# Optimization experiments

Measured on AMD Instinct MI355X. Metric: run time of the kernel, lower is better.

The kernel has to match this reference:

```python
import jax, jax.numpy as jnp
import numpy as np

LN_EPS = 1e-5      # torch.nn.LayerNorm default
NORM_EPS = 1e-12   # torch F.normalize default


def _layernorm(x, gamma, beta):
    mu = jnp.mean(x, axis=-1, keepdims=True)
    var = jnp.mean(jnp.square(x - mu), axis=-1, keepdims=True)
    return (x - mu) * jax.lax.rsqrt(var + LN_EPS) * gamma + beta


def _l2norm(x):
    # normalize over last (embedding) axis, matching F.normalize(dim=1) on [B,E,1,N]
    n = jnp.sqrt(jnp.sum(jnp.square(x), axis=-1, keepdims=True))
    return x / jnp.maximum(n, NORM_EPS)


def setup_inputs() -> dict:
    key = jax.random.key(0)
    ks = jax.random.split(key, 4)
    B, N, C, E = 8, 4096, 768, 768
    x = jax.random.normal(ks[0], (B, N, C), dtype=jnp.float32)
    w_qkv = jax.random.normal(ks[1], (C, 3 * E), dtype=jnp.float32) * (1.0 / np.sqrt(C))
    w_proj = jax.random.normal(ks[2], (E, C), dtype=jnp.float32) * (1.0 / np.sqrt(E))
    ln_in_g = jnp.ones((C,), jnp.float32)
    ln_in_b = jnp.zeros((C,), jnp.float32)
    ln_out_g = jnp.ones((E,), jnp.float32)
    ln_out_b = jnp.zeros((E,), jnp.float32)
    return {"x": x, "w_qkv": w_qkv, "w_proj": w_proj,
            "ln_in_g": ln_in_g, "ln_in_b": ln_in_b,
            "ln_out_g": ln_out_g, "ln_out_b": ln_out_b}


def reference(x, w_qkv, w_proj, ln_in_g, ln_in_b, ln_out_g, ln_out_b):
    # x: [B, N, C]
    h = _layernorm(x, ln_in_g, ln_in_b)
    qkv = h @ w_qkv                                  # [B, N, 3E]
    q, k, v = jnp.split(qkv, 3, axis=-1)             # each [B, N, E]
    phi_q = _l2norm(q)                               # per-token L2 over E
    phi_k = _l2norm(k)
    kv = jnp.sum(phi_k * v, axis=1)                  # [B, E] (sum over tokens N)
    attn = phi_q * kv[:, None, :]                    # [B, N, E]
    out = _layernorm(attn, ln_out_g, ln_out_b) @ w_proj  # [B, N, C]
    return out
```

## Files before the change

kernel.cpp:

```cpp
#include <hip/hip_runtime.h>
#include <hip/hip_bf16.h>
#include <cstdint>

typedef __bf16 bf16;
typedef __bf16 bf16x4 __attribute__((ext_vector_type(4)));
typedef __bf16 bf16x8 __attribute__((ext_vector_type(8)));
typedef float f32x4 __attribute__((ext_vector_type(4)));

#define GK 768
#define LN_EPS 1e-5f
#define NORM_EPS 1e-12f

__device__ __forceinline__ void gl_lds16(const void* g, void* l) {
  __builtin_amdgcn_global_load_lds(
      (__attribute__((address_space(1))) uint32_t*)(uintptr_t)g,
      (__attribute__((address_space(3))) uint32_t*)(uintptr_t)l,
      16, 0, 0);
}

__device__ __forceinline__ void blockReduce2w3(float& s, float& ss, float* sm) {
  #pragma unroll
  for (int o = 32; o > 0; o >>= 1) {
    s  += __shfl_down(s, o, 64);
    ss += __shfl_down(ss, o, 64);
  }
  int wave = threadIdx.x >> 6, lane = threadIdx.x & 63;
  if (lane == 0) { sm[wave] = s; sm[3 + wave] = ss; }
  __syncthreads();
  s  = sm[0] + sm[1] + sm[2];
  ss = sm[3] + sm[4] + sm[5];
  __syncthreads();
}

__global__ __launch_bounds__(256) void transpose_cvt(const float* __restrict__ w,
                                                     bf16* __restrict__ wt,
                                                     int R, int Ncols) {
  __shared__ float tile[32][33];
  int tx = threadIdx.x & 31, ty = threadIdx.x >> 5;
  int c0 = blockIdx.x * 32, r0 = blockIdx.y * 32;
  #pragma unroll
  for (int i = 0; i < 32; i += 8)
    tile[ty + i][tx] = w[(size_t)(r0 + ty + i) * Ncols + (c0 + tx)];
  __syncthreads();
  #pragma unroll
  for (int i = 0; i < 32; i += 8)
    wt[(size_t)(c0 + ty + i) * R + (r0 + tx)] = (bf16)tile[tx][ty + i];
}

__global__ __launch_bounds__(192) void ln_in_kernel(const float* __restrict__ x,
                                                    const float* __restrict__ g,
                                                    const float* __restrict__ b,
                                                    bf16* __restrict__ h) {
  __shared__ float sm[6];
  int row = blockIdx.x, t = threadIdx.x;
  const float* xr = x + (size_t)row * 768;
  float4 v = ((const float4*)xr)[t];
  float s  = v.x + v.y + v.z + v.w;
  float ss = v.x * v.x + v.y * v.y + v.z * v.z + v.w * v.w;
  blockReduce2w3(s, ss, sm);
  float mu  = s * (1.0f / 768.0f);
  float inv = rsqrtf(ss * (1.0f / 768.0f) - mu * mu + LN_EPS);
  float4 gg = ((const float4*)g)[t];
  float4 bb = ((const float4*)b)[t];
  bf16x4 o;
  o[0] = (bf16)((v.x - mu) * inv * gg.x + bb.x);
  o[1] = (bf16)((v.y - mu) * inv * gg.y + bb.y);
  o[2] = (bf16)((v.z - mu) * inv * gg.z + bb.z);
  o[3] = (bf16)((v.w - mu) * inv * gg.w + bb.w);
  ((bf16x4*)(h + (size_t)row * 768))[t] = o;
}


#define SWZ(x) ((x) ^ ((((x) >> 7) & 7) << 4))

#define BAR __builtin_amdgcn_s_barrier()
#define VMC(n) asm volatile("s_waitcnt vmcnt(" #n ")" ::: "memory")
#define PRIO1 __builtin_amdgcn_s_setprio(1)
#define PRIO0 __builtin_amdgcn_s_setprio(0)

#define LDA1(base, mh, i, ks) \
  af[i][ks] = *(const bf16x8*)((base) + SWZ((wm * 128 + ((mh) * 4 + (i)) * 16 + llo) * 128 + (ks) * 64 + lhi * 16))
#define RD_A(base, mh) do { \
  LDA1(base, mh, 0, 0); LDA1(base, mh, 1, 0); LDA1(base, mh, 2, 0); LDA1(base, mh, 3, 0); \
  LDA1(base, mh, 0, 1); LDA1(base, mh, 1, 1); LDA1(base, mh, 2, 1); LDA1(base, mh, 3, 1); } while (0)

#define LDB1(base, n, ks) \
  bf[n][ks] = *(const bf16x8*)((base) + SWZ(((((n) >> 1) * 128 + wn * 32 + ((n) & 1) * 16 + llo) * 128 + (ks) * 64 + lhi * 16)))
#define RD_B01(base) do { LDB1(base, 0, 0); LDB1(base, 1, 0); LDB1(base, 0, 1); LDB1(base, 1, 1); } while (0)
#define RD_B23(base) do { LDB1(base, 2, 0); LDB1(base, 3, 0); LDB1(base, 2, 1); LDB1(base, 3, 1); } while (0)

#define MF1(mh, nh, i, jn, ks) \
  acc[(mh) * 4 + (i)][(nh) * 2 + (jn)] = __builtin_amdgcn_mfma_f32_16x16x32_bf16( \
      af[i][ks], bf[(nh) * 2 + (jn)][ks], acc[(mh) * 4 + (i)][(nh) * 2 + (jn)], 0, 0, 0)
#define MF8(mh, nh, ks) do { \
  MF1(mh, nh, 0, 0, ks); MF1(mh, nh, 0, 1, ks); MF1(mh, nh, 1, 0, ks); MF1(mh, nh, 1, 1, ks); \
  MF1(mh, nh, 2, 0, ks); MF1(mh, nh, 2, 1, ks); MF1(mh, nh, 3, 0, ks); MF1(mh, nh, 3, 1, ks); } while (0)
#define MFQ(mh, nh) do { PRIO1; MF8(mh, nh, 0); MF8(mh, nh, 1); PRIO0; } while (0)

#define STA(b, q, kt) gl_lds16(A + srcA[q] + (kt) * 64, &As_[b][(q) * 4096 + wave * 512])
#define STB(b, q, kt) gl_lds16(Bt + srcB[q] + (kt) * 64, &Bs_[b][(q) * 4096 + wave * 512])

template <bool OUT_BF16>
__global__ __launch_bounds__(512, 2) void gemm8p(const bf16* __restrict__ A,
                                                 const bf16* __restrict__ Bt,
                                                 void* __restrict__ Cv,
                                                 int Nn, int NBN) {
  __shared__ __align__(16) bf16 As_[2][16384];
  __shared__ __align__(16) bf16 Bs_[2][16384];
  const int tid = threadIdx.x;
  const int wave = tid >> 6, lane = tid & 63;
  const int llo = lane & 15, lhi = lane >> 4;
  const int wm = wave >> 2, wn = wave & 3;

  const int nwg = gridDim.x, bid = blockIdx.x;
  const int wg = (bid & 7) * (nwg >> 3) + (bid >> 3);
  const int rb = wg / NBN, cb = wg - rb * NBN;
  const int brow = rb * 256, bcol = cb * 256;

  uint32_t srcA[4], srcB[4];
  #pragma unroll
  for (int q = 0; q < 4; ++q) {
    int d = q * 8192 + tid * 16;
    int a = SWZ(d);
    int r = a >> 7, c = (a & 127) >> 1;
    srcA[q] = (uint32_t)(brow + r) * GK + c;
    int nh = r >> 7, wnn = (r >> 5) & 3, r32 = r & 31;
    srcB[q] = (uint32_t)(bcol + wnn * 64 + nh * 32 + r32) * GK + c;
  }

  f32x4 acc[8][4];
  #pragma unroll
  for (int m = 0; m < 8; ++m)
    #pragma unroll
    for (int n = 0; n < 4; ++n) acc[m][n] = (f32x4){0.f, 0.f, 0.f, 0.f};

  bf16x8 af[4][2], bf[4][2];
  const char* As0 = (const char*)&As_[0][0];
  const char* As1 = (const char*)&As_[1][0];
  const char* Bs0 = (const char*)&Bs_[0][0];
  const char* Bs1 = (const char*)&Bs_[1][0];

  STA(0, 0, 0); STA(0, 1, 0); STA(0, 2, 0); STA(0, 3, 0);
  STB(0, 0, 0); STB(0, 1, 0); STB(0, 2, 0); STB(0, 3, 0);
  STA(1, 0, 1); STA(1, 2, 1); STB(1, 0, 1); STB(1, 1, 1);
  VMC(4);
  BAR;

  for (int j = 0; j < 6; ++j) {
    const int t1 = 2 * j + 1, t2 = 2 * j + 2, t3 = 2 * j + 3;
    RD_A(As0, 0); RD_B01(Bs0); RD_B23(Bs0);
    STA(1, 1, t1); STA(1, 3, t1);
    BAR;
    MFQ(0, 0);
    BAR;
    STB(1, 2, t1); STB(1, 3, t1);
    BAR;
    MFQ(0, 1);
    BAR;
    RD_A(As0, 1);
    STA(0, 0, t2); STA(0, 2, t2);
    BAR;
    MFQ(1, 0);
    BAR;
    STB(0, 0, t2); STB(0, 1, t2);
    BAR;
    MFQ(1, 1);
    VMC(4);
    BAR;
    RD_A(As1, 0); RD_B01(Bs1); RD_B23(Bs1);
    STA(0, 1, t2); STA(0, 3, t2);
    BAR;
    MFQ(0, 0);
    BAR;
    STB(0, 2, t2); STB(0, 3, t2);
    BAR;
    MFQ(0, 1);
    BAR;
    RD_A(As1, 1);
    STA(1, 0, t3); STA(1, 2, t3);
    BAR;
    MFQ(1, 0);
    BAR;
    STB(1, 0, t3); STB(1, 1, t3);
    BAR;
    MFQ(1, 1);
    VMC(4);
    BAR;
  }

  #pragma unroll
  for (int m = 0; m < 8; ++m) {
    #pragma unroll
    for (int n = 0; n < 4; ++n) {
      int row = brow + wm * 128 + m * 16 + lhi * 4;
      int col = bcol + wn * 64 + n * 16 + llo;
      #pragma unroll
      for (int r2 = 0; r2 < 4; ++r2) {
        if (OUT_BF16)
          ((bf16*)Cv)[(size_t)(row + r2) * Nn + col] = (bf16)acc[m][n][r2];
        else
          ((float*)Cv)[(size_t)(row + r2) * Nn + col] = acc[m][n][r2];
      }
    }
  }
}

__global__ __launch_bounds__(256) void kv_partial(const bf16* __restrict__ qkv,
                                                  float* __restrict__ kvp) {
  __shared__ float sm[4][768];
  int b = blockIdx.x >> 5, chunk = blockIdx.x & 31;
  int wave = threadIdx.x >> 6, lane = threadIdx.x & 63;
  const bf16* base = qkv + ((size_t)(b * 4096 + chunk * 128 + wave * 32)) * 2304;
  float acc[3][4] = {};
  for (int i = 0; i < 32; ++i) {
    const bf16* kr = base + (size_t)i * 2304 + 768;
    const bf16* vr = kr + 768;
    bf16x4 k4[3], v4[3];
    #pragma unroll
    for (int c = 0; c < 3; ++c) {
      k4[c] = *(const bf16x4*)(kr + c * 256 + lane * 4);
      v4[c] = *(const bf16x4*)(vr + c * 256 + lane * 4);
    }
    float ssk = 0.f;
    #pragma unroll
    for (int c = 0; c < 3; ++c)
      #pragma unroll
      for (int j = 0; j < 4; ++j) { float kf = (float)k4[c][j]; ssk += kf * kf; }
    #pragma unroll
    for (int off = 32; off > 0; off >>= 1) ssk += __shfl_xor(ssk, off, 64);
    float wi = 1.0f / fmaxf(sqrtf(ssk), NORM_EPS);
    #pragma unroll
    for (int c = 0; c < 3; ++c)
      #pragma unroll
      for (int j = 0; j < 4; ++j)
        acc[c][j] += (float)k4[c][j] * (float)v4[c][j] * wi;
  }
  #pragma unroll
  for (int c = 0; c < 3; ++c)
    #pragma unroll
    for (int j = 0; j < 4; ++j)
      sm[wave][c * 256 + lane * 4 + j] = acc[c][j];
  __syncthreads();
  int t = threadIdx.x;
  #pragma unroll
  for (int c = 0; c < 3; ++c) {
    int e = c * 256 + t;
    kvp[(size_t)blockIdx.x * 768 + e] = sm[0][e] + sm[1][e] + sm[2][e] + sm[3][e];
  }
}

__global__ __launch_bounds__(256) void kv_reduce(const float* __restrict__ kvp,
                                                 float* __restrict__ kv) {
  int i = blockIdx.x * 256 + threadIdx.x;
  int b = i / 768, e = i - b * 768;
  float s = 0.f;
  #pragma unroll
  for (int c = 0; c < 32; ++c) s += kvp[(size_t)(b * 32 + c) * 768 + e];
  kv[i] = s;
}

__global__ __launch_bounds__(192) void attn_ln_kernel(const bf16* __restrict__ qkv,
                                                      const float* __restrict__ kv,
                                                      const float* __restrict__ g,
                                                      const float* __restrict__ b,
                                                      bf16* __restrict__ a) {
  __shared__ float sm[6];
  int row = blockIdx.x, t = threadIdx.x;
  int bt = row >> 12;
  const bf16* qr = qkv + (size_t)row * 2304;
  bf16x4 q4 = ((const bf16x4*)qr)[t];
  float q0 = (float)q4[0], q1 = (float)q4[1], q2 = (float)q4[2], q3 = (float)q4[3];
  float sq = q0 * q0 + q1 * q1 + q2 * q2 + q3 * q3, dummy = 0.f;
  blockReduce2w3(sq, dummy, sm);
  float iq = 1.0f / fmaxf(sqrtf(sq), NORM_EPS);
  float4 kv4 = ((const float4*)(kv + bt * 768))[t];
  float4 av;
  av.x = q0 * iq * kv4.x;
  av.y = q1 * iq * kv4.y;
  av.z = q2 * iq * kv4.z;
  av.w = q3 * iq * kv4.w;
  float s  = av.x + av.y + av.z + av.w;
  float ss = av.x * av.x + av.y * av.y + av.z * av.z + av.w * av.w;
  blockReduce2w3(s, ss, sm);
  float mu  = s * (1.0f / 768.0f);
  float inv = rsqrtf(ss * (1.0f / 768.0f) - mu * mu + LN_EPS);
  float4 gg = ((const float4*)g)[t];
  float4 bb = ((const float4*)b)[t];
  bf16x4 o;
  o[0] = (bf16)((av.x - mu) * inv * gg.x + bb.x);
  o[1] = (bf16)((av.y - mu) * inv * gg.y + bb.y);
  o[2] = (bf16)((av.z - mu) * inv * gg.z + bb.z);
  o[3] = (bf16)((av.w - mu) * inv * gg.w + bb.w);
  ((bf16x4*)(a + (size_t)row * 768))[t] = o;
}

extern "C" void kernel_launch(void* const* d_in, const int* in_sizes, int n_in,
                              void* d_out, int out_size, void* d_ws, size_t ws_size,
                              hipStream_t stream) {
  const float* x      = (const float*)d_in[0];
  const float* w_qkv  = (const float*)d_in[1];
  const float* w_proj = (const float*)d_in[2];
  const float* g_in   = (const float*)d_in[3];
  const float* b_in   = (const float*)d_in[4];
  const float* g_out  = (const float*)d_in[5];
  const float* b_out  = (const float*)d_in[6];

  char* ws = (char*)d_ws;
  bf16*  wqkvt  = (bf16*)(ws);
  bf16*  wprojt = (bf16*)(ws + 3538944);
  bf16*  h      = (bf16*)(ws + 4718592);
  bf16*  qkv    = (bf16*)(ws + 55050240);
  float* kvp    = (float*)(ws + 206045184);
  float* kv     = (float*)(ws + 206831616);

  transpose_cvt<<<dim3(2304 / 32, 768 / 32), 256, 0, stream>>>(w_qkv, wqkvt, 768, 2304);
  transpose_cvt<<<dim3(768 / 32, 768 / 32), 256, 0, stream>>>(w_proj, wprojt, 768, 768);
  ln_in_kernel<<<32768, 192, 0, stream>>>(x, g_in, b_in, h);
  gemm8p<true><<<128 * 9, 512, 0, stream>>>(h, wqkvt, (void*)qkv, 2304, 9);
  kv_partial<<<256, 256, 0, stream>>>(qkv, kvp);
  kv_reduce<<<24, 256, 0, stream>>>(kvp, kv);
  attn_ln_kernel<<<32768, 192, 0, stream>>>(qkv, kv, g_out, b_out, h);
  gemm8p<false><<<128 * 3, 512, 0, stream>>>(h, wprojt, d_out, 768, 3);
}
```

Baseline: 292.3 us.

## Replace 256x256 GEMM tile with simpler 128x128 tile and double-buffered pipeline

Swaps the 512-thread 256x256-tile GEMM, with its finely interleaved quarter-step load/compute schedule, for a 256-thread 128x128-tile kernel. Each K-step reads all fragments, runs all 32 MFMAs, then stages the next full tile into the freed buffer. This gives a simpler schedule with fewer barriers and more workgroups for better CU fill. In exchange each tile gets less data reuse, so global and LDS traffic per FLOP rises, and load latency is less finely overlapped.

Result: faster. 268.9 us (-8.0%).

```diff
diff --git a/kernel.cpp b/kernel.cpp
--- a/kernel.cpp
+++ b/kernel.cpp
@@ -78,59 +78,65 @@
 #define PRIO1 __builtin_amdgcn_s_setprio(1)
 #define PRIO0 __builtin_amdgcn_s_setprio(0)
 
-#define LDA1(base, mh, i, ks) \
-  af[i][ks] = *(const bf16x8*)((base) + SWZ((wm * 128 + ((mh) * 4 + (i)) * 16 + llo) * 128 + (ks) * 64 + lhi * 16))
-#define RD_A(base, mh) do { \
-  LDA1(base, mh, 0, 0); LDA1(base, mh, 1, 0); LDA1(base, mh, 2, 0); LDA1(base, mh, 3, 0); \
-  LDA1(base, mh, 0, 1); LDA1(base, mh, 1, 1); LDA1(base, mh, 2, 1); LDA1(base, mh, 3, 1); } while (0)
-
-#define LDB1(base, n, ks) \
-  bf[n][ks] = *(const bf16x8*)((base) + SWZ(((((n) >> 1) * 128 + wn * 32 + ((n) & 1) * 16 + llo) * 128 + (ks) * 64 + lhi * 16)))
-#define RD_B01(base) do { LDB1(base, 0, 0); LDB1(base, 1, 0); LDB1(base, 0, 1); LDB1(base, 1, 1); } while (0)
-#define RD_B23(base) do { LDB1(base, 2, 0); LDB1(base, 3, 0); LDB1(base, 2, 1); LDB1(base, 3, 1); } while (0)
-
-#define MF1(mh, nh, i, jn, ks) \
-  acc[(mh) * 4 + (i)][(nh) * 2 + (jn)] = __builtin_amdgcn_mfma_f32_16x16x32_bf16( \
-      af[i][ks], bf[(nh) * 2 + (jn)][ks], acc[(mh) * 4 + (i)][(nh) * 2 + (jn)], 0, 0, 0)
-#define MF8(mh, nh, ks) do { \
-  MF1(mh, nh, 0, 0, ks); MF1(mh, nh, 0, 1, ks); MF1(mh, nh, 1, 0, ks); MF1(mh, nh, 1, 1, ks); \
-  MF1(mh, nh, 2, 0, ks); MF1(mh, nh, 2, 1, ks); MF1(mh, nh, 3, 0, ks); MF1(mh, nh, 3, 1, ks); } while (0)
-#define MFQ(mh, nh) do { PRIO1; MF8(mh, nh, 0); MF8(mh, nh, 1); PRIO0; } while (0)
-
-#define STA(b, q, kt) gl_lds16(A + srcA[q] + (kt) * 64, &As_[b][(q) * 4096 + wave * 512])
-#define STB(b, q, kt) gl_lds16(Bt + srcB[q] + (kt) * 64, &Bs_[b][(q) * 4096 + wave * 512])
+#define LDA1(base, i, ks) \
+  af[i][ks] = *(const bf16x8*)((base) + SWZ((wm * 64 + (i) * 16 + llo) * 128 + (ks) * 64 + lhi * 16))
+#define LDB1(base, j, ks) \
+  bf[j][ks] = *(const bf16x8*)((base) + SWZ((wn * 64 + (j) * 16 + llo) * 128 + (ks) * 64 + lhi * 16))
+#define RDALL(Ab, Bb) do { \
+  LDA1(Ab, 0, 0); LDA1(Ab, 1, 0); LDA1(Ab, 2, 0); LDA1(Ab, 3, 0); \
+  LDB1(Bb, 0, 0); LDB1(Bb, 1, 0); LDB1(Bb, 2, 0); LDB1(Bb, 3, 0); \
+  LDA1(Ab, 0, 1); LDA1(Ab, 1, 1); LDA1(Ab, 2, 1); LDA1(Ab, 3, 1); \
+  LDB1(Bb, 0, 1); LDB1(Bb, 1, 1); LDB1(Bb, 2, 1); LDB1(Bb, 3, 1); } while (0)
+
+#define MF1(m, n, ks) \
+  acc[m][n] = __builtin_amdgcn_mfma_f32_16x16x32_bf16(af[m][ks], bf[n][ks], acc[m][n], 0, 0, 0)
+#define MFALL do { PRIO1; \
+  MF1(0,0,0); MF1(0,1,0); MF1(0,2,0); MF1(0,3,0); \
+  MF1(1,0,0); MF1(1,1,0); MF1(1,2,0); MF1(1,3,0); \
+  MF1(2,0,0); MF1(2,1,0); MF1(2,2,0); MF1(2,3,0); \
+  MF1(3,0,0); MF1(3,1,0); MF1(3,2,0); MF1(3,3,0); \
+  MF1(0,0,1); MF1(0,1,1); MF1(0,2,1); MF1(0,3,1); \
+  MF1(1,0,1); MF1(1,1,1); MF1(1,2,1); MF1(1,3,1); \
+  MF1(2,0,1); MF1(2,1,1); MF1(2,2,1); MF1(2,3,1); \
+  MF1(3,0,1); MF1(3,1,1); MF1(3,2,1); MF1(3,3,1); \
+  PRIO0; } while (0)
+
+#define STA2(b, q, t) gl_lds16(A + srcA[q] + (t) * 64, &As_[b][(q) * 2048 + wave * 512])
+#define STB2(b, q, t) gl_lds16(Bt + srcB[q] + (t) * 64, &Bs_[b][(q) * 2048 + wave * 512])
+#define STAGE(b, t) do { \
+  STA2(b, 0, t); STA2(b, 1, t); STA2(b, 2, t); STA2(b, 3, t); \
+  STB2(b, 0, t); STB2(b, 1, t); STB2(b, 2, t); STB2(b, 3, t); } while (0)
 
 template <bool OUT_BF16>
-__global__ __launch_bounds__(512, 2) void gemm8p(const bf16* __restrict__ A,
-                                                 const bf16* __restrict__ Bt,
-                                                 void* __restrict__ Cv,
-                                                 int Nn, int NBN) {
-  __shared__ __align__(16) bf16 As_[2][16384];
-  __shared__ __align__(16) bf16 Bs_[2][16384];
+__global__ __launch_bounds__(256, 2) void gemm128(const bf16* __restrict__ A,
+                                                  const bf16* __restrict__ Bt,
+                                                  void* __restrict__ Cv,
+                                                  int Nn, int NBN) {
+  __shared__ __align__(16) bf16 As_[2][8192];
+  __shared__ __align__(16) bf16 Bs_[2][8192];
   const int tid = threadIdx.x;
   const int wave = tid >> 6, lane = tid & 63;
   const int llo = lane & 15, lhi = lane >> 4;
-  const int wm = wave >> 2, wn = wave & 3;
+  const int wm = wave >> 1, wn = wave & 1;
 
   const int nwg = gridDim.x, bid = blockIdx.x;
   const int wg = (bid & 7) * (nwg >> 3) + (bid >> 3);
   const int rb = wg / NBN, cb = wg - rb * NBN;
-  const int brow = rb * 256, bcol = cb * 256;
+  const int brow = rb * 128, bcol = cb * 128;
 
   uint32_t srcA[4], srcB[4];
   #pragma unroll
   for (int q = 0; q < 4; ++q) {
-    int d = q * 8192 + tid * 16;
+    int d = q * 4096 + tid * 16;
     int a = SWZ(d);
     int r = a >> 7, c = (a & 127) >> 1;
     srcA[q] = (uint32_t)(brow + r) * GK + c;
-    int nh = r >> 7, wnn = (r >> 5) & 3, r32 = r & 31;
-    srcB[q] = (uint32_t)(bcol + wnn * 64 + nh * 32 + r32) * GK + c;
-  }
-
-  f32x4 acc[8][4];
-  #pragma unroll
-  for (int m = 0; m < 8; ++m)
+    srcB[q] = (uint32_t)(bcol + r) * GK + c;
+  }
+
+  f32x4 acc[4][4];
+  #pragma unroll
+  for (int m = 0; m < 4; ++m)
     #pragma unroll
     for (int n = 0; n < 4; ++n) acc[m][n] = (f32x4){0.f, 0.f, 0.f, 0.f};
 
@@ -140,59 +146,39 @@
   const char* Bs0 = (const char*)&Bs_[0][0];
   const char* Bs1 = (const char*)&Bs_[1][0];
 
-  STA(0, 0, 0); STA(0, 1, 0); STA(0, 2, 0); STA(0, 3, 0);
-  STB(0, 0, 0); STB(0, 1, 0); STB(0, 2, 0); STB(0, 3, 0);
-  STA(1, 0, 1); STA(1, 2, 1); STB(1, 0, 1); STB(1, 1, 1);
-  VMC(4);
+  STAGE(0, 0);
+  STAGE(1, 1);
+  VMC(8);
   BAR;
 
-  for (int j = 0; j < 6; ++j) {
-    const int t1 = 2 * j + 1, t2 = 2 * j + 2, t3 = 2 * j + 3;
-    RD_A(As0, 0); RD_B01(Bs0); RD_B23(Bs0);
-    STA(1, 1, t1); STA(1, 3, t1);
+  #pragma unroll
+  for (int j = 0; j < 5; ++j) {
+    RDALL(As0, Bs0);
+    MFALL;
     BAR;
-    MFQ(0, 0);
+    STAGE(0, 2 * j + 2);
+    VMC(8);
     BAR;
-    STB(1, 2, t1); STB(1, 3, t1);
+    RDALL(As1, Bs1);
+    MFALL;
     BAR;
-    MFQ(0, 1);
+    STAGE(1, 2 * j + 3);
+    VMC(8);
     BAR;
-    RD_A(As0, 1);
-    STA(0, 0, t2); STA(0, 2, t2);
-    BAR;
-    MFQ(1, 0);
-    BAR;
-    STB(0, 0, t2); STB(0, 1, t2);
-    BAR;
-    MFQ(1, 1);
-    VMC(4);
-    BAR;
-    RD_A(As1, 0); RD_B01(Bs1); RD_B23(Bs1);
-    STA(0, 1, t2); STA(0, 3, t2);
-    BAR;
-    MFQ(0, 0);
-    BAR;
-    STB(0, 2, t2); STB(0, 3, t2);
-    BAR;
-    MFQ(0, 1);
-    BAR;
-    RD_A(As1, 1);
-    STA(1, 0, t3); STA(1, 2, t3);
-    BAR;
-    MFQ(1, 0);
-    BAR;
-    STB(1, 0, t3); STB(1, 1, t3);
-    BAR;
-    MFQ(1, 1);
-    VMC(4);
-    BAR;
-  }
-
-  #pragma unroll
-  for (int m = 0; m < 8; ++m) {
+  }
+  RDALL(As0, Bs0);
+  MFALL;
+  BAR;
+  VMC(0);
+  BAR;
+  RDALL(As1, Bs1);
+  MFALL;
+
+  #pragma unroll
+  for (int m = 0; m < 4; ++m) {
     #pragma unroll
     for (int n = 0; n < 4; ++n) {
-      int row = brow + wm * 128 + m * 16 + lhi * 4;
+      int row = brow + wm * 64 + m * 16 + lhi * 4;
       int col = bcol + wn * 64 + n * 16 + llo;
       #pragma unroll
       for (int r2 = 0; r2 < 4; ++r2) {
@@ -316,9 +302,9 @@
   transpose_cvt<<<dim3(2304 / 32, 768 / 32), 256, 0, stream>>>(w_qkv, wqkvt, 768, 2304);
   transpose_cvt<<<dim3(768 / 32, 768 / 32), 256, 0, stream>>>(w_proj, wprojt, 768, 768);
   ln_in_kernel<<<32768, 192, 0, stream>>>(x, g_in, b_in, h);
-  gemm8p<true><<<128 * 9, 512, 0, stream>>>(h, wqkvt, (void*)qkv, 2304, 9);
+  gemm128<true><<<256 * 18, 256, 0, stream>>>(h, wqkvt, (void*)qkv, 2304, 18);
   kv_partial<<<256, 256, 0, stream>>>(qkv, kvp);
   kv_reduce<<<24, 256, 0, stream>>>(kvp, kv);
   attn_ln_kernel<<<32768, 192, 0, stream>>>(qkv, kv, g_out, b_out, h);
-  gemm8p<false><<<128 * 3, 512, 0, stream>>>(h, wprojt, d_out, 768, 3);
-}
+  gemm128<false><<<256 * 6, 256, 0, stream>>>(h, wprojt, d_out, 768, 6);
+}
```
